# Performance work log

Hardware: AMD Instinct MI355X
Metric: run time of the kernel (lower is better)

Reference implementation:

```python
import jax, jax.numpy as jnp
import numpy as np

B, S, D, H = 2, 2048, 512, 8
HD = D // H
DFF = 4 * D
EPS_LN = 1e-5
EPS_ATTN = 1e-8


def layernorm(x, w, b):
    mu = jnp.mean(x, axis=-1, keepdims=True)
    var = jnp.var(x, axis=-1, keepdims=True)
    return (x - mu) * jax.lax.rsqrt(var + EPS_LN) * w + b


def masked_attention(q_src, v_src, wq, bq, wk, bk, wv, bv, wo, bo, M):
    # q_src/v_src: (B,S,D); M: (B,S,S)
    Bs, Ss, _ = q_src.shape
    Q = (q_src @ wq + bq).reshape(Bs, Ss, H, HD)
    K = (q_src @ wk + bk).reshape(Bs, Ss, H, HD)
    V = (v_src @ wv + bv).reshape(Bs, Ss, H, HD)
    scale = HD ** -0.5
    scores = jnp.einsum('bqhd,bkhd->bhqk', Q, K) * scale
    Mh = M[:, None, :, :]                      # (B,1,S,S) broadcast over heads
    scores = scores * Mh
    A = jax.nn.softmax(scores, axis=-1)
    A = A * Mh                                 # re-mask post-softmax
    A = A / (jnp.sum(jnp.abs(A), axis=-1, keepdims=True) + EPS_ATTN)  # L1 renorm
    out = jnp.einsum('bhqk,bkhd->bqhd', A, V).reshape(Bs, Ss, D)
    return out @ wo + bo


def ffn(x, w1, b1, w2, b2):
    h = jax.nn.gelu(x @ w1 + b1, approximate=False)
    return x + (h @ w2 + b2)                   # FeedForward(num_layers=2) includes residual


def setup_inputs() -> dict:
    key = jax.random.key(0)
    ks = iter(jax.random.split(key, 64))
    nrm = lambda shape, s=0.02: jax.random.normal(next(ks), shape, jnp.float32) * s
    d = {
        'gene_emb': jax.random.normal(next(ks), (B, S, D), jnp.float32),
        'expr_emb': jax.random.normal(next(ks), (B, S, D), jnp.float32),
        'M': jax.random.uniform(next(ks), (B, S, S), jnp.float32),
    }
    # gene attention params (weights stored (in,out))
    for p in ['g_wq', 'g_wk', 'g_wv', 'g_wo']:
        d[p] = nrm((D, D))
    for p in ['g_bq', 'g_bk', 'g_bv', 'g_bo']:
        d[p] = jnp.zeros((D,), jnp.float32)
    # expr attention params (fused proj 2D->D)
    d['e_wf'] = nrm((2 * D, D)); d['e_bf'] = jnp.zeros((D,), jnp.float32)
    for p in ['e_wq', 'e_wk', 'e_wv', 'e_wo']:
        d[p] = nrm((D, D))
    for p in ['e_bq', 'e_bk', 'e_bv', 'e_bo']:
        d[p] = jnp.zeros((D,), jnp.float32)
    # layernorms
    for p in ['ln_g1_w', 'ln_g2_w', 'ln_e1_w', 'ln_e2_w']:
        d[p] = jnp.ones((D,), jnp.float32)
    for p in ['ln_g1_b', 'ln_g2_b', 'ln_e1_b', 'ln_e2_b']:
        d[p] = jnp.zeros((D,), jnp.float32)
    # FFNs
    d['fg_w1'] = nrm((D, DFF)); d['fg_b1'] = jnp.zeros((DFF,), jnp.float32)
    d['fg_w2'] = nrm((DFF, D)); d['fg_b2'] = jnp.zeros((D,), jnp.float32)
    d['fe_w1'] = nrm((D, DFF)); d['fe_b1'] = jnp.zeros((DFF,), jnp.float32)
    d['fe_w2'] = nrm((DFF, D)); d['fe_b2'] = jnp.zeros((D,), jnp.float32)
    return d


def reference(gene_emb, expr_emb, M,
              g_wq, g_bq, g_wk, g_bk, g_wv, g_bv, g_wo, g_bo,
              e_wf, e_bf, e_wq, e_bq, e_wk, e_bk, e_wv, e_bv, e_wo, e_bo,
              ln_g1_w, ln_g1_b, ln_g2_w, ln_g2_b,
              ln_e1_w, ln_e1_b, ln_e2_w, ln_e2_b,
              fg_w1, fg_b1, fg_w2, fg_b2,
              fe_w1, fe_b1, fe_w2, fe_b2):
    # ----- gene branch -----
    xg = layernorm(gene_emb, ln_g1_w, ln_g1_b)
    attn_g = masked_attention(xg, xg, g_wq, g_bq, g_wk, g_bk, g_wv, g_bv, g_wo, g_bo, M)
    x = gene_emb + attn_g
    x_ln = layernorm(x, ln_g2_w, ln_g2_b)
    out_gene = x + ffn(x_ln, fg_w1, fg_b1, fg_w2, fg_b2)
    # ----- expression branch -----
    y_n = layernorm(expr_emb, ln_e1_w, ln_e1_b)
    fused = jnp.concatenate([gene_emb, y_n], axis=-1) @ e_wf + e_bf
    attn_e = masked_attention(fused, y_n, e_wq, e_bq, e_wk, e_bk, e_wv, e_bv, e_wo, e_bo, M)
    y = expr_emb + attn_e
    y_ln = layernorm(y, ln_e2_w, ln_e2_b)
    out_expr = y + ffn(y_ln, fe_w1, fe_b1, fe_w2, fe_b2)
    return (out_gene, out_expr)
```

## Files before the change

### kernel.cpp

```cpp
#include <hip/hip_runtime.h>
#include <math.h>

#define S_LEN 2048
#define DMODEL 512
#define NROWS 4096
#define NHEAD 8
#define HDIM 64
#define LOG2E 1.4426950408889634f

typedef __attribute__((ext_vector_type(8))) __bf16 bf16x8;
typedef __attribute__((ext_vector_type(4))) float f32x4;

__device__ inline float bf2f(unsigned short h) {
    unsigned u = ((unsigned)h) << 16;
    return __builtin_bit_cast(float, u);
}
__device__ inline unsigned short f2bf(float f) {
    unsigned u = __builtin_bit_cast(unsigned, f);
    return (unsigned short)((u + 0x7fffu + ((u >> 16) & 1u)) >> 16);
}

__device__ inline void gl_lds16(const unsigned short* g, unsigned short* l) {
    __builtin_amdgcn_global_load_lds(
        (const __attribute__((address_space(1))) void*)g,
        (__attribute__((address_space(3))) void*)l, 16, 0, 0);
}

__global__ __launch_bounds__(256) void wcast_t(
    const float* __restrict__ W, unsigned short* __restrict__ Wt, int K, int Mo)
{
    __shared__ float t[32][33];
    const int bx = blockIdx.x * 32;
    const int by = blockIdx.y * 32;
    const int tx = threadIdx.x & 31, ty = threadIdx.x >> 5;
    #pragma unroll
    for (int r = 0; r < 4; ++r)
        t[ty + 8 * r][tx] = W[(size_t)(by + ty + 8 * r) * Mo + bx + tx];
    __syncthreads();
    #pragma unroll
    for (int r = 0; r < 4; ++r)
        Wt[(size_t)(bx + ty + 8 * r) * K + by + tx] = f2bf(t[tx][ty + 8 * r]);
}

__global__ __launch_bounds__(256) void wcast_sq8(
    const float* w0, const float* w1, const float* w2, const float* w3,
    const float* w4, const float* w5, const float* w6, const float* w7,
    unsigned short* __restrict__ dst)
{
    const float* srcs[8] = {w0, w1, w2, w3, w4, w5, w6, w7};
    const float* __restrict__ W = srcs[blockIdx.z];
    unsigned short* __restrict__ Wt = dst + (size_t)blockIdx.z * 512 * 512;
    __shared__ float t[32][33];
    const int bx = blockIdx.x * 32, by = blockIdx.y * 32;
    const int tx = threadIdx.x & 31, ty = threadIdx.x >> 5;
    #pragma unroll
    for (int r = 0; r < 4; ++r)
        t[ty + 8 * r][tx] = W[(size_t)(by + ty + 8 * r) * 512 + bx + tx];
    __syncthreads();
    #pragma unroll
    for (int r = 0; r < 4; ++r)
        Wt[(size_t)(bx + ty + 8 * r) * 512 + by + tx] = f2bf(t[tx][ty + 8 * r]);
}

__global__ __launch_bounds__(256) void wcast_t2(
    const float* wA, const float* wB, unsigned short* __restrict__ dst,
    int K, int Mo)
{
    const float* __restrict__ W = blockIdx.z ? wB : wA;
    unsigned short* __restrict__ Wt = dst + (size_t)blockIdx.z * K * Mo;
    __shared__ float t[32][33];
    const int bx = blockIdx.x * 32, by = blockIdx.y * 32;
    const int tx = threadIdx.x & 31, ty = threadIdx.x >> 5;
    #pragma unroll
    for (int r = 0; r < 4; ++r)
        t[ty + 8 * r][tx] = W[(size_t)(by + ty + 8 * r) * Mo + bx + tx];
    __syncthreads();
    #pragma unroll
    for (int r = 0; r < 4; ++r)
        Wt[(size_t)(bx + ty + 8 * r) * K + by + tx] = f2bf(t[tx][ty + 8 * r]);
}

__global__ __launch_bounds__(256) void pack_bias(
    const float* __restrict__ b1, const float* __restrict__ b2,
    const float* __restrict__ b3, float* __restrict__ dst, int n)
{
    int t = blockIdx.x * 256 + threadIdx.x;
    if (t >= n) return;
    float v = (t < 512) ? b1[t] : (t < 1024) ? b2[t - 512] : b3[t - 1024];
    dst[t] = v;
}

__global__ __launch_bounds__(256) void cast_strided(
    const float* __restrict__ in, unsigned short* __restrict__ out, int ostride)
{
    const int row = blockIdx.x, t = threadIdx.x;
    out[(size_t)row * ostride + t]       = f2bf(in[(size_t)row * DMODEL + t]);
    out[(size_t)row * ostride + t + 256] = f2bf(in[(size_t)row * DMODEL + t + 256]);
}

__global__ __launch_bounds__(256) void ln_kernel(
    const float* __restrict__ x, const float* __restrict__ w,
    const float* __restrict__ b, unsigned short* __restrict__ y, int ostride)
{
    __shared__ float red[8];
    const int row = blockIdx.x;
    const float* xr = x + (size_t)row * DMODEL;
    const int t = threadIdx.x;
    float v0 = xr[t];
    float v1 = xr[t + 256];
    float s  = v0 + v1;
    float sq = v0 * v0 + v1 * v1;
    #pragma unroll
    for (int o = 32; o > 0; o >>= 1) {
        s  += __shfl_down(s, o);
        sq += __shfl_down(sq, o);
    }
    int wid = t >> 6, lane = t & 63;
    if (lane == 0) { red[wid] = s; red[4 + wid] = sq; }
    __syncthreads();
    float mean = (red[0] + red[1] + red[2] + red[3]) * (1.0f / 512.0f);
    float msq  = (red[4] + red[5] + red[6] + red[7]) * (1.0f / 512.0f);
    float var  = msq - mean * mean;
    float rs   = rsqrtf(var + 1e-5f);
    y[(size_t)row * ostride + t]       = f2bf((v0 - mean) * rs * w[t] + b[t]);
    y[(size_t)row * ostride + t + 256] = f2bf((v1 - mean) * rs * w[t + 256] + b[t + 256]);
}

__global__ __launch_bounds__(256) void vtrans(
    const unsigned short* __restrict__ V, int ldv, unsigned short* __restrict__ Vt)
{
    __shared__ unsigned short t[64][72];
    const int s0 = blockIdx.x * 64, h = blockIdx.y, b = blockIdx.z;
    const int tid = threadIdx.x;
    {
        const int r = tid >> 2, c = (tid & 3) * 16;
        const unsigned short* src = V + (size_t)(b * S_LEN + s0 + r) * ldv + h * 64 + c;
        *(int4*)&t[r][c]     = *(const int4*)(src);
        *(int4*)&t[r][c + 8] = *(const int4*)(src + 8);
    }
    __syncthreads();
    {
        const int d = tid >> 2, s = (tid & 3) * 16;
        unsigned short* dst = Vt + ((size_t)((b * 8 + h) * 64 + d)) * S_LEN + s0 + s;
        unsigned short tmp[16];
        #pragma unroll
        for (int e = 0; e < 16; ++e) tmp[e] = t[s + e][d];
        *(int4*)dst       = *(int4*)&tmp[0];
        *(int4*)(dst + 8) = *(int4*)&tmp[8];
    }
}

__global__ __launch_bounds__(256) void gemm_mfma(
    const unsigned short* __restrict__ A, int lda,
    const unsigned short* __restrict__ Bt,
    const float* __restrict__ bias,
    const float* __restrict__ R1,
    const unsigned short* __restrict__ R2,
    float* __restrict__ Cf, unsigned short* __restrict__ Cb,
    int K, int Mo, int dogelu)
{
    __shared__ __align__(16) unsigned short As[128 * 32];
    __shared__ __align__(16) unsigned short Bs[128 * 32];
    const int tid = threadIdx.x;
    const int wave = tid >> 6, lane = tid & 63;
    const int wr = wave >> 1, wc = wave & 1;
    const int row0 = blockIdx.y * 128, col0 = blockIdx.x * 128;
    const int l15 = lane & 15, q = lane >> 4;

    f32x4 acc[4][4];
    const f32x4 zz = {0.f, 0.f, 0.f, 0.f};
    #pragma unroll
    for (int i = 0; i < 4; ++i)
        #pragma unroll
        for (int j = 0; j < 4; ++j) acc[i][j] = zz;

    for (int k0 = 0; k0 < K; k0 += 32) {
        #pragma unroll
        for (int r = 0; r < 2; ++r) {
            int idx = r * 256 + tid;
            int row = idx >> 2, kc = idx & 3;
            gl_lds16(&A[(size_t)(row0 + row) * lda + k0 + kc * 8],
                     &As[(size_t)(r * 256 + wave * 64) * 8]);
            gl_lds16(&Bt[(size_t)(col0 + row) * K + k0 + kc * 8],
                     &Bs[(size_t)(r * 256 + wave * 64) * 8]);
        }
        __syncthreads();
        bf16x8 af[4], bfr[4];
        #pragma unroll
        for (int fi = 0; fi < 4; ++fi)
            af[fi] = *(const bf16x8*)&As[(wr * 64 + fi * 16 + l15) * 32 + q * 8];
        #pragma unroll
        for (int fj = 0; fj < 4; ++fj)
            bfr[fj] = *(const bf16x8*)&Bs[(wc * 64 + fj * 16 + l15) * 32 + q * 8];
        #pragma unroll
        for (int fi = 0; fi < 4; ++fi)
            #pragma unroll
            for (int fj = 0; fj < 4; ++fj)
                acc[fi][fj] = __builtin_amdgcn_mfma_f32_16x16x32_bf16(
                    af[fi], bfr[fj], acc[fi][fj], 0, 0, 0);
        __syncthreads();
    }

    #pragma unroll
    for (int fi = 0; fi < 4; ++fi) {
        #pragma unroll
        for (int reg = 0; reg < 4; ++reg) {
            int row = row0 + wr * 64 + fi * 16 + q * 4 + reg;
            #pragma unroll
            for (int fj = 0; fj < 4; ++fj) {
                int col = col0 + wc * 64 + fj * 16 + l15;
                float v = acc[fi][fj][reg] + bias[col];
                if (dogelu) v = 0.5f * v * (1.0f + erff(v * 0.70710678118654752f));
                size_t off = (size_t)row * Mo + col;
                if (R1) v += R1[off];
                if (R2) v += bf2f(R2[off]);
                if (Cb) Cb[off] = f2bf(v);
                else    Cf[off] = v;
            }
        }
    }
}

__global__ __launch_bounds__(256) void gemm_mfma64(
    const unsigned short* __restrict__ A, int lda,
    const unsigned short* __restrict__ Bt,
    const float* __restrict__ bias,
    const float* __restrict__ R1,
    const unsigned short* __restrict__ R2,
    float* __restrict__ Cf, unsigned short* __restrict__ Cb,
    int K, int Mo, int dogelu)
{
    __shared__ __align__(16) unsigned short As[64 * 64];
    __shared__ __align__(16) unsigned short Bs[64 * 64];
    const int tid = threadIdx.x;
    const int wave = tid >> 6, lane = tid & 63;
    const int row0 = blockIdx.y * 64, col0 = blockIdx.x * 64;
    const int l15 = lane & 15, q = lane >> 4;

    f32x4 acc[4];
    const f32x4 zz = {0.f, 0.f, 0.f, 0.f};
    #pragma unroll
    for (int j = 0; j < 4; ++j) acc[j] = zz;

    for (int k0 = 0; k0 < K; k0 += 64) {
        #pragma unroll
        for (int r = 0; r < 2; ++r) {
            int idx = r * 256 + tid;
            int row = idx >> 3, kc = idx & 7;
            gl_lds16(&A[(size_t)(row0 + row) * lda + k0 + kc * 8],
                     &As[(size_t)(r * 256 + wave * 64) * 8]);
            gl_lds16(&Bt[(size_t)(col0 + row) * K + k0 + kc * 8],
                     &Bs[(size_t)(r * 256 + wave * 64) * 8]);
        }
        __syncthreads();
        #pragma unroll
        for (int ks = 0; ks < 2; ++ks) {
            bf16x8 af = *(const bf16x8*)&As[(wave * 16 + l15) * 64 + ks * 32 + q * 8];
            bf16x8 bfr[4];
            #pragma unroll
            for (int fj = 0; fj < 4; ++fj)
                bfr[fj] = *(const bf16x8*)&Bs[(fj * 16 + l15) * 64 + ks * 32 + q * 8];
            #pragma unroll
            for (int fj = 0; fj < 4; ++fj)
                acc[fj] = __builtin_amdgcn_mfma_f32_16x16x32_bf16(af, bfr[fj], acc[fj], 0, 0, 0);
        }
        __syncthreads();
    }

    #pragma unroll
    for (int reg = 0; reg < 4; ++reg) {
        int row = row0 + wave * 16 + q * 4 + reg;
        #pragma unroll
        for (int fj = 0; fj < 4; ++fj) {
            int col = col0 + fj * 16 + l15;
            float v = acc[fj][reg] + bias[col];
            if (dogelu) v = 0.5f * v * (1.0f + erff(v * 0.70710678118654752f));
            size_t off = (size_t)row * Mo + col;
            if (R1) v += R1[off];
            if (R2) v += bf2f(R2[off]);
            if (Cb) Cb[off] = f2bf(v);
            else    Cf[off] = v;
        }
    }
}

__global__ __launch_bounds__(256, 4) void attn_mfma_split(
    const unsigned short* __restrict__ Q, int ldq,
    const unsigned short* __restrict__ Kp, int ldk,
    const unsigned short* __restrict__ Vt,
    const float* __restrict__ M,
    unsigned short* __restrict__ Opart,
    float* __restrict__ stats)
{
    __shared__ __align__(16) unsigned short Ks[64 * 72];
    __shared__ __align__(16) unsigned short Vs[64 * 72];
    __shared__ __align__(16) unsigned short Ps_all[4][16 * 72];

    const int bh = blockIdx.y, b = bh >> 3, h = bh & 7;
    const int q0 = blockIdx.x * 64;
    const int p = blockIdx.z;
    const int tid = threadIdx.x, wave = tid >> 6, lane = tid & 63;
    const int l15 = lane & 15, quad = lane >> 4;
    const int iRow = q0 + wave * 16 + l15;
    const int kBeg = p * (S_LEN / 2), kEnd = kBeg + (S_LEN / 2);

    unsigned short* Ps = &Ps_all[wave][0];

    bf16x8 qf[2];
    {
        const unsigned short* qp = Q + (size_t)(b * S_LEN + iRow) * ldq + h * HDIM + quad * 8;
        #pragma unroll
        for (int ks = 0; ks < 2; ++ks) {
            union { bf16x8 v; unsigned short u[8]; } tq;
            tq.v = *(const bf16x8*)(qp + ks * 32);
            #pragma unroll
            for (int e = 0; e < 8; ++e)
                tq.u[e] = f2bf(bf2f(tq.u[e]) * (0.125f * LOG2E));
            qf[ks] = tq.v;
        }
    }

    const int srow = tid >> 3;
    const int scol = (tid & 7) * 8;
    const unsigned short* kg = Kp + ((size_t)b * S_LEN) * ldk + h * HDIM + scol;
    const unsigned short* vg = Vt + ((size_t)bh * 64 + srow) * S_LEN + scol;
    const float* mrow = M + ((size_t)b * S_LEN + iRow) * S_LEN + quad * 4;

    float rm = -INFINITY, rZ = 0.f, rZm = 0.f;
    f32x4 oacc[4];
    const f32x4 zz = {0.f, 0.f, 0.f, 0.f};
    #pragma unroll
    for (int dt = 0; dt < 4; ++dt) oacc[dt] = zz;

    int4 kv0 = *(const int4*)(kg + (size_t)(kBeg + srow) * ldk);
    int4 kv1 = *(const int4*)(kg + (size_t)(kBeg + srow + 32) * ldk);
    int4 vv0 = *(const int4*)(vg + kBeg);
    int4 vv1 = *(const int4*)(vg + 32 * S_LEN + kBeg);
    *(int4*)&Ks[srow * 72 + scol]        = kv0;
    *(int4*)&Ks[(srow + 32) * 72 + scol] = kv1;
    *(int4*)&Vs[srow * 72 + scol]        = vv0;
    *(int4*)&Vs[(srow + 32) * 72 + scol] = vv1;
    __syncthreads();

    for (int k0 = kBeg; k0 < kEnd; k0 += 64) {
        const bool more = (k0 + 64 < kEnd);
        if (more) {
            kv0 = *(const int4*)(kg + (size_t)(k0 + 64 + srow) * ldk);
            kv1 = *(const int4*)(kg + (size_t)(k0 + 64 + srow + 32) * ldk);
            vv0 = *(const int4*)(vg + k0 + 64);
            vv1 = *(const int4*)(vg + 32 * S_LEN + k0 + 64);
        }
        float4 m4[4];
        #pragma unroll
        for (int jt = 0; jt < 4; ++jt)
            m4[jt] = *(const float4*)(mrow + k0 + jt * 16);

        f32x4 sacc[4];
        #pragma unroll
        for (int jt = 0; jt < 4; ++jt) sacc[jt] = zz;
        __builtin_amdgcn_s_setprio(1);
        #pragma unroll
        for (int jt = 0; jt < 4; ++jt) {
            bf16x8 kf0 = *(const bf16x8*)&Ks[(jt * 16 + l15) * 72 + quad * 8];
            bf16x8 kf1 = *(const bf16x8*)&Ks[(jt * 16 + l15) * 72 + 32 + quad * 8];
            sacc[jt] = __builtin_amdgcn_mfma_f32_16x16x32_bf16(kf0, qf[0], sacc[jt], 0, 0, 0);
            sacc[jt] = __builtin_amdgcn_mfma_f32_16x16x32_bf16(kf1, qf[1], sacc[jt], 0, 0, 0);
        }
        __builtin_amdgcn_s_setprio(0);

        float mx = -INFINITY;
        #pragma unroll
        for (int jt = 0; jt < 4; ++jt) {
            float mm[4] = {m4[jt].x, m4[jt].y, m4[jt].z, m4[jt].w};
            #pragma unroll
            for (int r = 0; r < 4; ++r) {
                sacc[jt][r] = sacc[jt][r] * mm[r];
                mx = fmaxf(mx, sacc[jt][r]);
            }
        }
        mx = fmaxf(mx, __shfl_xor(mx, 16));
        mx = fmaxf(mx, __shfl_xor(mx, 32));
        if (!__all(mx <= rm + 8.0f)) {
            float mn = fmaxf(rm, mx);
            float al = __builtin_amdgcn_exp2f(rm - mn);
            rm = mn; rZ *= al; rZm *= al;
            #pragma unroll
            for (int dt = 0; dt < 4; ++dt)
                #pragma unroll
                for (int r = 0; r < 4; ++r) oacc[dt][r] *= al;
        }

        float z = 0.f, zm = 0.f;
        #pragma unroll
        for (int jt = 0; jt < 4; ++jt) {
            float mm[4] = {m4[jt].x, m4[jt].y, m4[jt].z, m4[jt].w};
            float pv[4];
            #pragma unroll
            for (int r = 0; r < 4; ++r) {
                float e = __builtin_amdgcn_exp2f(sacc[jt][r] - rm);
                float pm = e * mm[r];
                z += e; zm += pm; pv[r] = pm;
            }
            unsigned lo, hi;
            asm("v_cvt_pk_bf16_f32 %0, %1, %2" : "=v"(lo) : "v"(pv[0]), "v"(pv[1]));
            asm("v_cvt_pk_bf16_f32 %0, %1, %2" : "=v"(hi) : "v"(pv[2]), "v"(pv[3]));
            uint2 pk; pk.x = lo; pk.y = hi;
            *(uint2*)&Ps[l15 * 72 + jt * 16 + quad * 4] = pk;
        }
        z  += __shfl_xor(z, 16);  z  += __shfl_xor(z, 32);
        zm += __shfl_xor(zm, 16); zm += __shfl_xor(zm, 32);
        rZ += z; rZm += zm;

        bf16x8 pf0 = *(const bf16x8*)&Ps[l15 * 72 + quad * 8];
        bf16x8 pf1 = *(const bf16x8*)&Ps[l15 * 72 + 32 + quad * 8];
        __builtin_amdgcn_s_setprio(1);
        #pragma unroll
        for (int dt = 0; dt < 4; ++dt) {
            bf16x8 vf0 = *(const bf16x8*)&Vs[(dt * 16 + l15) * 72 + quad * 8];
            bf16x8 vf1 = *(const bf16x8*)&Vs[(dt * 16 + l15) * 72 + 32 + quad * 8];
            oacc[dt] = __builtin_amdgcn_mfma_f32_16x16x32_bf16(vf0, pf0, oacc[dt], 0, 0, 0);
            oacc[dt] = __builtin_amdgcn_mfma_f32_16x16x32_bf16(vf1, pf1, oacc[dt], 0, 0, 0);
        }
        __builtin_amdgcn_s_setprio(0);

        if (more) {
            __syncthreads();
            *(int4*)&Ks[srow * 72 + scol]        = kv0;
            *(int4*)&Ks[(srow + 32) * 72 + scol] = kv1;
            *(int4*)&Vs[srow * 72 + scol]        = vv0;
            *(int4*)&Vs[(srow + 32) * 72 + scol] = vv1;
            __syncthreads();
        }
    }

    unsigned short* op = Opart + (((size_t)(p * 16 + bh) * S_LEN + iRow) * 64);
    #pragma unroll
    for (int dt = 0; dt < 4; ++dt) {
        unsigned lo, hi;
        asm("v_cvt_pk_bf16_f32 %0, %1, %2" : "=v"(lo) : "v"(oacc[dt][0]), "v"(oacc[dt][1]));
        asm("v_cvt_pk_bf16_f32 %0, %1, %2" : "=v"(hi) : "v"(oacc[dt][2]), "v"(oacc[dt][3]));
        uint2 o2; o2.x = lo; o2.y = hi;
        *(uint2*)(op + dt * 16 + quad * 4) = o2;
    }
    if (quad == 0) {
        float4 st; st.x = rm; st.y = rZ; st.z = rZm; st.w = 0.f;
        *(float4*)&stats[(((size_t)p * 16 + bh) * S_LEN + iRow) * 4] = st;
    }
}

__global__ __launch_bounds__(256) void attn_combine(
    const unsigned short* __restrict__ Opart, const float* __restrict__ stats,
    unsigned short* __restrict__ O)
{
    const int bh = blockIdx.y, b = bh >> 3, h = bh & 7;
    const int q0 = blockIdx.x * 64;
    const int tid = threadIdx.x;
    const int i = tid >> 2, dq = (tid & 3) * 16;
    const int qg = q0 + i;

    float4 s0 = *(const float4*)&stats[(((size_t)0 * 16 + bh) * S_LEN + qg) * 4];
    float4 s1 = *(const float4*)&stats[(((size_t)1 * 16 + bh) * S_LEN + qg) * 4];
    float ms = fmaxf(s0.x, s1.x);
    float w0 = __builtin_amdgcn_exp2f(s0.x - ms), w1 = __builtin_amdgcn_exp2f(s1.x - ms);
    float Z  = w0 * s0.y + w1 * s1.y;
    float Zm = w0 * s0.z + w1 * s1.z;
    float inv = 1.0f / (Zm + 1e-8f * Z);
    w0 *= inv; w1 *= inv;

    const unsigned short* p0 = Opart + (((size_t)0 * 16 + bh) * S_LEN + qg) * 64 + dq;
    const unsigned short* p1 = Opart + (((size_t)1 * 16 + bh) * S_LEN + qg) * 64 + dq;
    union { int4 v; unsigned short u[8]; } a0, a1, r;
    unsigned short* dst = O + (size_t)(b * S_LEN + qg) * DMODEL + h * HDIM + dq;
    #pragma unroll
    for (int half = 0; half < 2; ++half) {
        a0.v = *(const int4*)(p0 + half * 8);
        a1.v = *(const int4*)(p1 + half * 8);
        #pragma unroll
        for (int e = 0; e < 8; ++e)
            r.u[e] = f2bf(w0 * bf2f(a0.u[e]) + w1 * bf2f(a1.u[e]));
        *(int4*)(dst + half * 8) = r.v;
    }
}

extern "C" void kernel_launch(void* const* d_in, const int* in_sizes, int n_in,
                              void* d_out, int out_size, void* d_ws, size_t ws_size,
                              hipStream_t stream)
{
    const float* gene_emb = (const float*)d_in[0];
    const float* expr_emb = (const float*)d_in[1];
    const float* M        = (const float*)d_in[2];
    const float* g_wq = (const float*)d_in[3];
    const float* g_wk = (const float*)d_in[4];
    const float* g_wv = (const float*)d_in[5];
    const float* g_wo = (const float*)d_in[6];
    const float* g_bq = (const float*)d_in[7];
    const float* g_bk = (const float*)d_in[8];
    const float* g_bv = (const float*)d_in[9];
    const float* g_bo = (const float*)d_in[10];
    const float* e_wf = (const float*)d_in[11];
    const float* e_bf = (const float*)d_in[12];
    const float* e_wq = (const float*)d_in[13];
    const float* e_wk = (const float*)d_in[14];
    const float* e_wv = (const float*)d_in[15];
    const float* e_wo = (const float*)d_in[16];
    const float* e_bq = (const float*)d_in[17];
    const float* e_bk = (const float*)d_in[18];
    const float* e_bv = (const float*)d_in[19];
    const float* e_bo = (const float*)d_in[20];
    const float* ln_g1_w = (const float*)d_in[21];
    const float* ln_g2_w = (const float*)d_in[22];
    const float* ln_e1_w = (const float*)d_in[23];
    const float* ln_e2_w = (const float*)d_in[24];
    const float* ln_g1_b = (const float*)d_in[25];
    const float* ln_g2_b = (const float*)d_in[26];
    const float* ln_e1_b = (const float*)d_in[27];
    const float* ln_e2_b = (const float*)d_in[28];
    const float* fg_w1 = (const float*)d_in[29];
    const float* fg_b1 = (const float*)d_in[30];
    const float* fg_w2 = (const float*)d_in[31];
    const float* fg_b2 = (const float*)d_in[32];
    const float* fe_w1 = (const float*)d_in[33];
    const float* fe_b1 = (const float*)d_in[34];
    const float* fe_w2 = (const float*)d_in[35];
    const float* fe_b2 = (const float*)d_in[36];

    float* out_gene = (float*)d_out;
    float* out_expr = out_gene + (size_t)NROWS * DMODEL;

    char* ws = (char*)d_ws;
    const size_t MB1 = 1024 * 1024;
    unsigned short* bufA16  = (unsigned short*)(ws + 0 * MB1);
    unsigned short* bufAt16 = (unsigned short*)(ws + 4 * MB1);
    unsigned short* bufQKV  = (unsigned short*)(ws + 8 * MB1);
    unsigned short* bufQKe  = (unsigned short*)(ws + 8 * MB1);
    unsigned short* bufV16  = (unsigned short*)(ws + 16 * MB1);
    unsigned short* bufVt   = (unsigned short*)(ws + 20 * MB1);
    unsigned short* bufCat  = (unsigned short*)(ws + 24 * MB1);
    unsigned short* bufOp   = (unsigned short*)(ws + 24 * MB1);
    float*          bufSt   = (float*)(ws + 32 * MB1);
    float*          bufX    = (float*)(ws + 33 * MB1);
    unsigned short* bufH16  = (unsigned short*)(ws + 8 * MB1);
    char* wp = ws + 41 * MB1;
    unsigned short* sq8    = (unsigned short*)wp;
    unsigned short* gwq_t  = sq8 + 0 * 512 * 512;
    unsigned short* gwk_t  = sq8 + 1 * 512 * 512;
    unsigned short* gwv_t  = sq8 + 2 * 512 * 512;
    unsigned short* gwo_t  = sq8 + 3 * 512 * 512;
    unsigned short* ewq_t  = sq8 + 4 * 512 * 512;
    unsigned short* ewk_t  = sq8 + 5 * 512 * 512;
    unsigned short* ewv_t  = sq8 + 6 * 512 * 512;
    unsigned short* ewo_t  = sq8 + 7 * 512 * 512;
    unsigned short* ewf_t  = sq8 + 8 * 512 * 512;
    unsigned short* ffn1   = ewf_t + 1024 * 512;
    unsigned short* fgw1_t = ffn1;
    unsigned short* few1_t = ffn1 + 512 * 2048;
    unsigned short* ffn2   = few1_t + 512 * 2048;
    unsigned short* fgw2_t = ffn2;
    unsigned short* few2_t = ffn2 + 2048 * 512;
    float* biasg = (float*)(few2_t + 2048 * 512);
    float* biase = biasg + 1536;

    dim3 blk(256);
    dim3 ln_grid(NROWS);
    dim3 g512s(8, 64);
    dim3 g1024(8, 32);
    dim3 g1536(12, 32);
    dim3 g2048(16, 32);
    dim3 attn_grid(S_LEN / 64, 16, 2);
    dim3 comb_grid(S_LEN / 64, 16);
    dim3 vt_grid(S_LEN / 64, NHEAD, 2);

    wcast_sq8<<<dim3(16, 16, 8), blk, 0, stream>>>(
        g_wq, g_wk, g_wv, g_wo, e_wq, e_wk, e_wv, e_wo, sq8);
    wcast_t<<<dim3(16, 32), blk, 0, stream>>>(e_wf, ewf_t, 1024, 512);
    wcast_t2<<<dim3(64, 16, 2), blk, 0, stream>>>(fg_w1, fe_w1, ffn1, 512, 2048);
    wcast_t2<<<dim3(16, 64, 2), blk, 0, stream>>>(fg_w2, fe_w2, ffn2, 2048, 512);
    pack_bias<<<dim3(6), blk, 0, stream>>>(g_bq, g_bk, g_bv, biasg, 1536);
    pack_bias<<<dim3(4), blk, 0, stream>>>(e_bq, e_bk, e_bk, biase, 1024);

    ln_kernel<<<ln_grid, blk, 0, stream>>>(gene_emb, ln_g1_w, ln_g1_b, bufA16, 512);
    gemm_mfma<<<g1536, blk, 0, stream>>>(bufA16, 512, gwq_t, biasg, nullptr, nullptr, nullptr, bufQKV, 512, 1536, 0);
    vtrans<<<vt_grid, blk, 0, stream>>>(bufQKV + 1024, 1536, bufVt);
    attn_mfma_split<<<attn_grid, blk, 0, stream>>>(bufQKV, 1536, bufQKV + 512, 1536, bufVt, M, bufOp, bufSt);
    attn_combine<<<comb_grid, blk, 0, stream>>>(bufOp, bufSt, bufAt16);
    gemm_mfma64<<<g512s, blk, 0, stream>>>(bufAt16, 512, gwo_t, g_bo, gene_emb, nullptr, bufX, nullptr, 512, 512, 0);
    ln_kernel<<<ln_grid, blk, 0, stream>>>(bufX, ln_g2_w, ln_g2_b, bufA16, 512);
    gemm_mfma<<<g2048, blk, 0, stream>>>(bufA16, 512, fgw1_t, fg_b1, nullptr, nullptr, nullptr, bufH16, 512, 2048, 1);
    gemm_mfma64<<<g512s, blk, 0, stream>>>(bufH16, 2048, fgw2_t, fg_b2, bufX, bufA16, out_gene, nullptr, 2048, 512, 0);

    cast_strided<<<ln_grid, blk, 0, stream>>>(gene_emb, bufCat, 1024);
    ln_kernel<<<ln_grid, blk, 0, stream>>>(expr_emb, ln_e1_w, ln_e1_b, bufCat + 512, 1024);
    gemm_mfma64<<<g512s, blk, 0, stream>>>(bufCat, 1024, ewf_t, e_bf, nullptr, nullptr, nullptr, bufA16, 1024, 512, 0);
    gemm_mfma<<<g1024, blk, 0, stream>>>(bufA16, 512, ewq_t, biase, nullptr, nullptr, nullptr, bufQKe, 512, 1024, 0);
    gemm_mfma64<<<g512s, blk, 0, stream>>>(bufCat + 512, 1024, ewv_t, e_bv, nullptr, nullptr, nullptr, bufV16, 512, 512, 0);
    vtrans<<<vt_grid, blk, 0, stream>>>(bufV16, 512, bufVt);
    attn_mfma_split<<<attn_grid, blk, 0, stream>>>(bufQKe, 1024, bufQKe + 512, 1024, bufVt, M, bufOp, bufSt);
    attn_combine<<<comb_grid, blk, 0, stream>>>(bufOp, bufSt, bufAt16);
    gemm_mfma64<<<g512s, blk, 0, stream>>>(bufAt16, 512, ewo_t, e_bo, expr_emb, nullptr, bufX, nullptr, 512, 512, 0);
    ln_kernel<<<ln_grid, blk, 0, stream>>>(bufX, ln_e2_w, ln_e2_b, bufA16, 512);
    gemm_mfma<<<g2048, blk, 0, stream>>>(bufA16, 512, few1_t, fe_b1, nullptr, nullptr, nullptr, bufH16, 512, 2048, 1);
    gemm_mfma64<<<g512s, blk, 0, stream>>>(bufH16, 2048, few2_t, fe_b2, bufX, bufA16, out_expr, nullptr, 2048, 512, 0);
}
```

Measured before the change: 539.1 us.

## Triple-buffer GEMM loads, swizzle LDS, fuse LN+cast, defer attention row-sum shuffles

```diff
diff --git a/kernel.cpp b/kernel.cpp
--- a/kernel.cpp
+++ b/kernel.cpp
@@ -88,14 +88,6 @@
     if (t >= n) return;
     float v = (t < 512) ? b1[t] : (t < 1024) ? b2[t - 512] : b3[t - 1024];
     dst[t] = v;
-}
-
-__global__ __launch_bounds__(256) void cast_strided(
-    const float* __restrict__ in, unsigned short* __restrict__ out, int ostride)
-{
-    const int row = blockIdx.x, t = threadIdx.x;
-    out[(size_t)row * ostride + t]       = f2bf(in[(size_t)row * DMODEL + t]);
-    out[(size_t)row * ostride + t + 256] = f2bf(in[(size_t)row * DMODEL + t + 256]);
 }
 
 __global__ __launch_bounds__(256) void ln_kernel(
@@ -126,6 +118,39 @@
     y[(size_t)row * ostride + t + 256] = f2bf((v1 - mean) * rs * w[t + 256] + b[t + 256]);
 }
 
+__global__ __launch_bounds__(256) void ln_cat_kernel(
+    const float* __restrict__ xg, const float* __restrict__ xe,
+    const float* __restrict__ w, const float* __restrict__ b,
+    unsigned short* __restrict__ y)
+{
+    __shared__ float red[8];
+    const int row = blockIdx.x;
+    const int t = threadIdx.x;
+    const float* gr = xg + (size_t)row * DMODEL;
+    const float* er = xe + (size_t)row * DMODEL;
+    float g0 = gr[t], g1 = gr[t + 256];
+    float v0 = er[t], v1 = er[t + 256];
+    float s  = v0 + v1;
+    float sq = v0 * v0 + v1 * v1;
+    #pragma unroll
+    for (int o = 32; o > 0; o >>= 1) {
+        s  += __shfl_down(s, o);
+        sq += __shfl_down(sq, o);
+    }
+    int wid = t >> 6, lane = t & 63;
+    if (lane == 0) { red[wid] = s; red[4 + wid] = sq; }
+    __syncthreads();
+    float mean = (red[0] + red[1] + red[2] + red[3]) * (1.0f / 512.0f);
+    float msq  = (red[4] + red[5] + red[6] + red[7]) * (1.0f / 512.0f);
+    float var  = msq - mean * mean;
+    float rs   = rsqrtf(var + 1e-5f);
+    unsigned short* yr = y + (size_t)row * 1024;
+    yr[t]             = f2bf(g0);
+    yr[t + 256]       = f2bf(g1);
+    yr[512 + t]       = f2bf((v0 - mean) * rs * w[t] + b[t]);
+    yr[512 + t + 256] = f2bf((v1 - mean) * rs * w[t + 256] + b[t + 256]);
+}
+
 __global__ __launch_bounds__(256) void vtrans(
     const unsigned short* __restrict__ V, int ldv, unsigned short* __restrict__ Vt)
 {
@@ -159,8 +184,8 @@
     float* __restrict__ Cf, unsigned short* __restrict__ Cb,
     int K, int Mo, int dogelu)
 {
-    __shared__ __align__(16) unsigned short As[128 * 32];
-    __shared__ __align__(16) unsigned short Bs[128 * 32];
+    __shared__ __align__(16) unsigned short As[3][128 * 32];
+    __shared__ __align__(16) unsigned short Bs[3][128 * 32];
     const int tid = threadIdx.x;
     const int wave = tid >> 6, lane = tid & 63;
     const int wr = wave >> 1, wc = wave & 1;
@@ -174,31 +199,45 @@
         #pragma unroll
         for (int j = 0; j < 4; ++j) acc[i][j] = zz;
 
-    for (int k0 = 0; k0 < K; k0 += 32) {
+    const int nk = K >> 5;
+    auto stage = [&](int t, int buf) {
+        const int k0 = t * 32;
         #pragma unroll
         for (int r = 0; r < 2; ++r) {
             int idx = r * 256 + tid;
             int row = idx >> 2, kc = idx & 3;
             gl_lds16(&A[(size_t)(row0 + row) * lda + k0 + kc * 8],
-                     &As[(size_t)(r * 256 + wave * 64) * 8]);
+                     &As[buf][(size_t)(r * 256 + wave * 64) * 8]);
             gl_lds16(&Bt[(size_t)(col0 + row) * K + k0 + kc * 8],
-                     &Bs[(size_t)(r * 256 + wave * 64) * 8]);
-        }
-        __syncthreads();
+                     &Bs[buf][(size_t)(r * 256 + wave * 64) * 8]);
+        }
+    };
+    stage(0, 0);
+    if (nk > 1) stage(1, 1);
+
+    int cur = 0, nx2 = 2;
+    for (int t = 0; t < nk; ++t) {
+        if (t + 1 < nk) asm volatile("s_waitcnt vmcnt(4)" ::: "memory");
+        else            asm volatile("s_waitcnt vmcnt(0)" ::: "memory");
+        __builtin_amdgcn_s_barrier();
+        if (t + 2 < nk) stage(t + 2, nx2);
+
         bf16x8 af[4], bfr[4];
         #pragma unroll
         for (int fi = 0; fi < 4; ++fi)
-            af[fi] = *(const bf16x8*)&As[(wr * 64 + fi * 16 + l15) * 32 + q * 8];
+            af[fi] = *(const bf16x8*)&As[cur][(wr * 64 + fi * 16 + l15) * 32 + q * 8];
         #pragma unroll
         for (int fj = 0; fj < 4; ++fj)
-            bfr[fj] = *(const bf16x8*)&Bs[(wc * 64 + fj * 16 + l15) * 32 + q * 8];
+            bfr[fj] = *(const bf16x8*)&Bs[cur][(wc * 64 + fj * 16 + l15) * 32 + q * 8];
         #pragma unroll
         for (int fi = 0; fi < 4; ++fi)
             #pragma unroll
             for (int fj = 0; fj < 4; ++fj)
                 acc[fi][fj] = __builtin_amdgcn_mfma_f32_16x16x32_bf16(
                     af[fi], bfr[fj], acc[fi][fj], 0, 0, 0);
-        __syncthreads();
+
+        cur = (cur == 2) ? 0 : cur + 1;
+        nx2 = (nx2 == 2) ? 0 : nx2 + 1;
     }
 
     #pragma unroll
@@ -230,8 +269,8 @@
     float* __restrict__ Cf, unsigned short* __restrict__ Cb,
     int K, int Mo, int dogelu)
 {
-    __shared__ __align__(16) unsigned short As[64 * 64];
-    __shared__ __align__(16) unsigned short Bs[64 * 64];
+    __shared__ __align__(16) unsigned short As[3][64 * 64];
+    __shared__ __align__(16) unsigned short Bs[3][64 * 64];
     const int tid = threadIdx.x;
     const int wave = tid >> 6, lane = tid & 63;
     const int row0 = blockIdx.y * 64, col0 = blockIdx.x * 64;
@@ -242,29 +281,45 @@
     #pragma unroll
     for (int j = 0; j < 4; ++j) acc[j] = zz;
 
-    for (int k0 = 0; k0 < K; k0 += 64) {
+    const int nk = K >> 6;
+    auto stage = [&](int t, int buf) {
+        const int k0 = t * 64;
         #pragma unroll
         for (int r = 0; r < 2; ++r) {
             int idx = r * 256 + tid;
-            int row = idx >> 3, kc = idx & 7;
+            int row = idx >> 3;
+            int kc  = (idx & 7) ^ (row & 7);
             gl_lds16(&A[(size_t)(row0 + row) * lda + k0 + kc * 8],
-                     &As[(size_t)(r * 256 + wave * 64) * 8]);
+                     &As[buf][(size_t)(r * 256 + wave * 64) * 8]);
             gl_lds16(&Bt[(size_t)(col0 + row) * K + k0 + kc * 8],
-                     &Bs[(size_t)(r * 256 + wave * 64) * 8]);
-        }
-        __syncthreads();
+                     &Bs[buf][(size_t)(r * 256 + wave * 64) * 8]);
+        }
+    };
+    stage(0, 0);
+    if (nk > 1) stage(1, 1);
+
+    int cur = 0, nx2 = 2;
+    for (int t = 0; t < nk; ++t) {
+        if (t + 1 < nk) asm volatile("s_waitcnt vmcnt(4)" ::: "memory");
+        else            asm volatile("s_waitcnt vmcnt(0)" ::: "memory");
+        __builtin_amdgcn_s_barrier();
+        if (t + 2 < nk) stage(t + 2, nx2);
+
         #pragma unroll
         for (int ks = 0; ks < 2; ++ks) {
-            bf16x8 af = *(const bf16x8*)&As[(wave * 16 + l15) * 64 + ks * 32 + q * 8];
+            const int cx = ((ks * 4 + q) ^ (l15 & 7)) * 8;
+            bf16x8 af = *(const bf16x8*)&As[cur][(wave * 16 + l15) * 64 + cx];
             bf16x8 bfr[4];
             #pragma unroll
             for (int fj = 0; fj < 4; ++fj)
-                bfr[fj] = *(const bf16x8*)&Bs[(fj * 16 + l15) * 64 + ks * 32 + q * 8];
+                bfr[fj] = *(const bf16x8*)&Bs[cur][(fj * 16 + l15) * 64 + cx];
             #pragma unroll
             for (int fj = 0; fj < 4; ++fj)
                 acc[fj] = __builtin_amdgcn_mfma_f32_16x16x32_bf16(af, bfr[fj], acc[fj], 0, 0, 0);
         }
-        __syncthreads();
+
+        cur = (cur == 2) ? 0 : cur + 1;
+        nx2 = (nx2 == 2) ? 0 : nx2 + 1;
     }
 
     #pragma unroll
@@ -368,16 +423,17 @@
         }
         __builtin_amdgcn_s_setprio(0);
 
-        float mx = -INFINITY;
+        float mxj[4];
         #pragma unroll
         for (int jt = 0; jt < 4; ++jt) {
             float mm[4] = {m4[jt].x, m4[jt].y, m4[jt].z, m4[jt].w};
             #pragma unroll
-            for (int r = 0; r < 4; ++r) {
+            for (int r = 0; r < 4; ++r)
                 sacc[jt][r] = sacc[jt][r] * mm[r];
-                mx = fmaxf(mx, sacc[jt][r]);
-            }
-        }
+            mxj[jt] = fmaxf(fmaxf(sacc[jt][0], sacc[jt][1]),
+                            fmaxf(sacc[jt][2], sacc[jt][3]));
+        }
+        float mx = fmaxf(fmaxf(mxj[0], mxj[1]), fmaxf(mxj[2], mxj[3]));
         mx = fmaxf(mx, __shfl_xor(mx, 16));
         mx = fmaxf(mx, __shfl_xor(mx, 32));
         if (!__all(mx <= rm + 8.0f)) {
@@ -407,8 +463,6 @@
             uint2 pk; pk.x = lo; pk.y = hi;
             *(uint2*)&Ps[l15 * 72 + jt * 16 + quad * 4] = pk;
         }
-        z  += __shfl_xor(z, 16);  z  += __shfl_xor(z, 32);
-        zm += __shfl_xor(zm, 16); zm += __shfl_xor(zm, 32);
         rZ += z; rZm += zm;
 
         bf16x8 pf0 = *(const bf16x8*)&Ps[l15 * 72 + quad * 8];
@@ -432,6 +486,9 @@
             __syncthreads();
         }
     }
+
+    rZ  += __shfl_xor(rZ, 16);  rZ  += __shfl_xor(rZ, 32);
+    rZm += __shfl_xor(rZm, 16); rZm += __shfl_xor(rZm, 32);
 
     unsigned short* op = Opart + (((size_t)(p * 16 + bh) * S_LEN + iRow) * 64);
     #pragma unroll
@@ -588,8 +645,7 @@
     gemm_mfma<<<g2048, blk, 0, stream>>>(bufA16, 512, fgw1_t, fg_b1, nullptr, nullptr, nullptr, bufH16, 512, 2048, 1);
     gemm_mfma64<<<g512s, blk, 0, stream>>>(bufH16, 2048, fgw2_t, fg_b2, bufX, bufA16, out_gene, nullptr, 2048, 512, 0);
 
-    cast_strided<<<ln_grid, blk, 0, stream>>>(gene_emb, bufCat, 1024);
-    ln_kernel<<<ln_grid, blk, 0, stream>>>(expr_emb, ln_e1_w, ln_e1_b, bufCat + 512, 1024);
+    ln_cat_kernel<<<ln_grid, blk, 0, stream>>>(gene_emb, expr_emb, ln_e1_w, ln_e1_b, bufCat);
     gemm_mfma64<<<g512s, blk, 0, stream>>>(bufCat, 1024, ewf_t, e_bf, nullptr, nullptr, nullptr, bufA16, 1024, 512, 0);
     gemm_mfma<<<g1024, blk, 0, stream>>>(bufA16, 512, ewq_t, biase, nullptr, nullptr, nullptr, bufQKe, 512, 1024, 0);
     gemm_mfma64<<<g512s, blk, 0, stream>>>(bufCat + 512, 1024, ewv_t, e_bv, nullptr, nullptr, nullptr, bufV16, 512, 512, 0);
```

Result: faster. 520.8 us (-3.4%).
